# Kernel optimization log

Measured on AMD Instinct MI355X. Metric: run time of the kernel, lower is better.

Reference implementation:

```python
import jax, jax.numpy as jnp
import numpy as np

B, DIM, H, W = 2, 256, 64, 64
HEADS, DIM_HEAD = 8, 64
DIM_INNER = HEADS * DIM_HEAD  # 512


def setup_inputs() -> dict:
    key = jax.random.key(0)
    k1, k2, k3 = jax.random.split(key, 3)
    fmap = jax.random.normal(k1, (B, DIM, H, W), dtype=jnp.float32)
    # 1x1 convs == channel matmuls; store as [out_ch, in_ch]
    w_qkv = jax.random.normal(k2, (3 * DIM_INNER, DIM), dtype=jnp.float32) * (DIM ** -0.5)
    w_out = jax.random.normal(k3, (DIM, DIM_INNER), dtype=jnp.float32) * (DIM_INNER ** -0.5)
    return {"fmap": fmap, "w_qkv": w_qkv, "w_out": w_out}


def reference(fmap, w_qkv, w_out):
    b, c, x, y = fmap.shape
    n = x * y
    h, d = HEADS, DIM_HEAD
    xt = fmap.reshape(b, c, n)                       # [B, C, N]
    qkv = jnp.einsum('oc,bcn->bon', w_qkv, xt)        # [B, 3*h*d, N]
    q, k, v = jnp.split(qkv, 3, axis=1)               # each [B, h*d, N]
    # -> [B, h, N, d]
    to_bhnd = lambda t: t.reshape(b, h, d, n).transpose(0, 1, 3, 2)
    q, k, v = to_bhnd(q), to_bhnd(k), to_bhnd(v)
    # Euclidean distance matrix (torch.cdist p=2)
    q2 = jnp.sum(q * q, axis=-1)                      # [B, h, N]
    k2 = jnp.sum(k * k, axis=-1)                      # [B, h, N]
    qk = jnp.einsum('bhid,bhjd->bhij', q, k)          # [B, h, N, N]
    sim = jnp.sqrt(jnp.maximum(q2[..., :, None] + k2[..., None, :] - 2.0 * qk, 0.0))
    attn = jax.nn.softmax(sim, axis=-1)
    out = jnp.einsum('bhij,bhjd->bhid', attn, v)      # [B, h, N, d]
    out = out.transpose(0, 1, 3, 2).reshape(b, h * d, n)  # [B, h*d, N]
    out = jnp.einsum('oc,bcn->bon', w_out, out)       # [B, dim, N]
    return out.reshape(b, c, x, y)
```

## Files before the change

kernel.cpp:

```cpp
#include <hip/hip_runtime.h>

#define B_      2
#define DIM_    256
#define N_      4096
#define HEADS_  8
#define DINNER_ 512

typedef _Float16 half_t;
typedef _Float16 half8  __attribute__((ext_vector_type(8)));
typedef _Float16 half4v __attribute__((ext_vector_type(4)));
typedef _Float16 half2v __attribute__((ext_vector_type(2)));
typedef float    floatx4 __attribute__((ext_vector_type(4)));

#define SCL_    1.4426950408889634f
#define SHIFT2_ 20.0f


__global__ __launch_bounds__(256) void prep_all(const float* __restrict__ fmap,
                                                const float* __restrict__ w_qkv,
                                                const float* __restrict__ w_out,
                                                half_t* __restrict__ wqF,
                                                half_t* __restrict__ woF,
                                                half_t* __restrict__ xTg) {
    const int t = threadIdx.x, bx = blockIdx.x;
    __shared__ float Tl[64 * 68];
    if (bx < 96) {
        half_t* dst = wqF + (size_t)bx * 4096;
#pragma unroll
        for (int j = 0; j < 2; ++j) {
            const int cch = j * 256 + t;
            const int o = cch >> 4, m15 = cch & 15;
            const float4 a  = *(const float4*)&w_qkv[(size_t)(bx * 16 + m15) * 256 + o * 8];
            const float4 bb = *(const float4*)&w_qkv[(size_t)(bx * 16 + m15) * 256 + o * 8 + 4];
            half8 hv;
            hv[0] = (half_t)a.x;  hv[1] = (half_t)a.y;  hv[2] = (half_t)a.z;  hv[3] = (half_t)a.w;
            hv[4] = (half_t)bb.x; hv[5] = (half_t)bb.y; hv[6] = (half_t)bb.z; hv[7] = (half_t)bb.w;
            *(half8*)(dst + o * 128 + m15 * 8) = hv;
        }
    } else if (bx < 112) {
        const int mt = bx - 96;
        half_t* dst = woF + (size_t)mt * 8192;
#pragma unroll
        for (int j = 0; j < 4; ++j) {
            const int cch = j * 256 + t;
            const int o = cch >> 4, m15 = cch & 15;
            const float4 a  = *(const float4*)&w_out[(size_t)(mt * 16 + m15) * 512 + o * 8];
            const float4 bb = *(const float4*)&w_out[(size_t)(mt * 16 + m15) * 512 + o * 8 + 4];
            half8 hv;
            hv[0] = (half_t)a.x;  hv[1] = (half_t)a.y;  hv[2] = (half_t)a.z;  hv[3] = (half_t)a.w;
            hv[4] = (half_t)bb.x; hv[5] = (half_t)bb.y; hv[6] = (half_t)bb.z; hv[7] = (half_t)bb.w;
            *(half8*)(dst + o * 128 + m15 * 8) = hv;
        }
    } else {
        const int idx = bx - 112;
        const int n0 = (idx & 63) * 64, k0 = ((idx >> 6) & 3) * 64, b = idx >> 8;
        {
            const int kk = t >> 2, nq = (t & 3) * 16;
#pragma unroll
            for (int q = 0; q < 4; ++q) {
                float4 v = *(const float4*)&fmap[((size_t)b * DIM_ + k0 + kk) * N_ + n0 + nq + 4 * q];
                *(float4*)&Tl[kk * 68 + nq + 4 * q] = v;
            }
        }
        __syncthreads();
        {
            const int n = t >> 2, ko = (t & 3) * 16;
            half8 h0, h1;
#pragma unroll
            for (int j = 0; j < 8; ++j) h0[j] = (half_t)Tl[(ko + j) * 68 + n];
#pragma unroll
            for (int j = 0; j < 8; ++j) h1[j] = (half_t)Tl[(ko + 8 + j) * 68 + n];
            half_t* dst = xTg + (((size_t)b * 64 + (n0 >> 6)) * 4 + (k0 >> 6)) * 4096;
            const int o0 = ((ko >> 5) * 4 + (n >> 4)) * 512 + (((ko >> 3) & 3) * 16 + (n & 15)) * 8;
            const int k8 = ko + 8;
            const int o1 = ((k8 >> 5) * 4 + (n >> 4)) * 512 + (((k8 >> 3) & 3) * 16 + (n & 15)) * 8;
            *(half8*)(dst + o0) = h0;
            *(half8*)(dst + o1) = h1;
        }
    }
}

__global__ __launch_bounds__(256) void mm_qkv_mf(const half_t* __restrict__ wqF,
                                                 const half_t* __restrict__ xTg,
                                                 half_t* __restrict__ perm,
                                                 float* __restrict__ sq) {
    const int nt64 = blockIdx.x, by = blockIdx.y, b = blockIdx.z;
    const int t = threadIdx.x, w = t >> 6, L = t & 63, c = L & 15, g = L >> 4;
    const int mt = by * 4 + w;

    const half_t* Ab = wqF + (size_t)mt * 4096;
    const half_t* Bb = xTg + (((size_t)b * 64 + nt64) * 4) * 4096;

    __shared__ __align__(16) char smraw[8192 + 4352];
    half_t* VtH = (half_t*)smraw;
    float*  red = (float*)(smraw + 8192);

    const floatx4 fz = {0.f, 0.f, 0.f, 0.f};
    floatx4 acc[4];
#pragma unroll
    for (int ns = 0; ns < 4; ++ns) acc[ns] = fz;

#pragma unroll
    for (int kc = 0; kc < 8; ++kc) {
        const half8 af = *(const half8*)(Ab + (kc * 4 + g) * 128 + c * 8);
        const half_t* Bs = Bb + (kc >> 1) * 4096 + (kc & 1) * 2048;
#pragma unroll
        for (int ns = 0; ns < 4; ++ns) {
            const half8 bf = *(const half8*)(Bs + ns * 512 + L * 8);
            acc[ns] = __builtin_amdgcn_mfma_f32_16x16x32_f16(af, bf, acc[ns], 0, 0, 0);
        }
    }

    half_t* dst = perm + (((size_t)(b * 24 + by) * 64 + nt64) << 12);
    if (by < 16) {
        float part[4];
#pragma unroll
        for (int ns = 0; ns < 4; ++ns) {
            half_t hv[4];
            float s = 0.f;
#pragma unroll
            for (int i = 0; i < 4; ++i) {
                hv[i] = (half_t)(acc[ns][i] * SCL_);
                const float f = (float)hv[i];
                s = fmaf(f, f, s);
            }
            part[ns] = s;
            const int off = ((w >> 1) * 4 + ns) * 512 + (((2 * w + (g >> 1)) & 3) * 16 + c) * 8 + 4 * (g & 1);
            half2v p0, p1;
            p0[0] = hv[0]; p0[1] = hv[1];
            p1[0] = hv[2]; p1[1] = hv[3];
            *(half2v*)(VtH + off)     = p0;
            *(half2v*)(VtH + off + 2) = p1;
        }
#pragma unroll
        for (int ns = 0; ns < 4; ++ns)
            red[(ns * 16 + (w * 4 + g)) * 17 + c] = part[ns];
        __syncthreads();
#pragma unroll
        for (int j = 0; j < 2; ++j)
            *(half8*)(dst + t * 16 + j * 8) = *(half8*)(VtH + t * 16 + j * 8);
        if (t < 64) {
            const int ns = t >> 4, cc = t & 15;
            float s = 0.f;
#pragma unroll
            for (int wg = 0; wg < 16; ++wg) s += red[(ns * 16 + wg) * 17 + cc];
            const int tens = by >> 3, hh = by & 7;
            sq[((size_t)(tens * 16 + b * 8 + hh)) * N_ + nt64 * 64 + ns * 16 + cc] = s;
        }
    } else {
#pragma unroll
        for (int ns = 0; ns < 4; ++ns)
#pragma unroll
            for (int i = 0; i < 4; ++i)
                VtH[(ns * 4 + w) * 256 + ((c >> 2) * 16 + 4 * g + i) * 4 + (c & 3)] = (half_t)acc[ns][i];
        __syncthreads();
#pragma unroll
        for (int j = 0; j < 2; ++j)
            *(half8*)(dst + t * 16 + j * 8) = *(half8*)(VtH + t * 16 + j * 8);
    }
}

__global__ __launch_bounds__(512) void attn_mfma(const half_t* __restrict__ perm,
                                                 const float* __restrict__ sq,
                                                 half_t* __restrict__ oh,
                                                 float* __restrict__ lbuf) {
    const int bx = blockIdx.x;
    const int qb = bx & 15, kh = bx >> 4;
    const int h = blockIdx.y, b = blockIdx.z;
    const int bh = b * HEADS_ + h;

    const half_t* Qb = perm + ((size_t)(b * 24 + h) << 18);
    const half_t* Kb = perm + ((size_t)(b * 24 + 8 + h) << 18);
    const half_t* Vb = perm + ((size_t)(b * 24 + 16 + h) << 18);
    const float* q2a = sq + (size_t)bh * N_;
    const float* k2a = sq + (size_t)(16 + bh) * N_;

    __shared__ __align__(16) half_t Kl[2][4096];
    __shared__ __align__(16) half_t Vl[2][4096];
    __shared__ __align__(16) float  k2l[1024];

    const int t = threadIdx.x, w = t >> 6, L = t & 63, c = L & 15, g = L >> 4;
    const floatx4 fz = {0.f, 0.f, 0.f, 0.f};

    *(float2*)&k2l[t * 2] = *(const float2*)&k2a[kh * 1024 + t * 2];

    const int tl = w >> 1;
    const int p0 = (w & 1) * 2, p1 = p0 + 1;
    const half_t* Qt = Qb + ((size_t)(qb * 4 + tl) << 12);
    const half8 bq0a = *(const half8*)(Qt + (0 * 4 + p0) * 512 + L * 8);
    const half8 bq1a = *(const half8*)(Qt + (1 * 4 + p0) * 512 + L * 8);
    const half8 bq0b = *(const half8*)(Qt + (0 * 4 + p1) * 512 + L * 8);
    const half8 bq1b = *(const half8*)(Qt + (1 * 4 + p1) * 512 + L * 8);
    const float q2la = q2a[qb * 256 + 64 * tl + 16 * p0 + c];
    const float q2lb = q2a[qb * 256 + 64 * tl + 16 * p1 + c];

    half4v aone;
    {
        const half_t ov = (c == 0) ? (half_t)1.0f : (half_t)0.0f;
        aone[0] = ov; aone[1] = ov; aone[2] = ov; aone[3] = ov;
    }

    floatx4 Oa[4], Ob[4];
    floatx4 laca = fz, lacb = fz;
#pragma unroll
    for (int dt = 0; dt < 4; ++dt) { Oa[dt] = fz; Ob[dt] = fz; }

    const int kt0 = kh * 16;
    half8 rk = *(const half8*)(Kb + ((size_t)kt0 << 12) + t * 8);
    half8 rv = *(const half8*)(Vb + ((size_t)kt0 << 12) + t * 8);

    for (int it = 0; it < 16; ++it) {
        const int buf = it & 1;
        *(half8*)(&Kl[buf][t * 8]) = rk;
        *(half8*)(&Vl[buf][t * 8]) = rv;
        asm volatile("s_waitcnt lgkmcnt(0)\n\ts_barrier" ::: "memory");
        if (it < 15) {
            rk = *(const half8*)(Kb + ((size_t)(kt0 + it + 1) << 12) + t * 8);
            rv = *(const half8*)(Vb + ((size_t)(kt0 + it + 1) << 12) + t * 8);
        }

#pragma unroll
        for (int nt = 0; nt < 4; ++nt) {
            const half8 ak0 = *(const half8*)(&Kl[buf][(0 * 4 + nt) * 512 + L * 8]);
            const half8 ak1 = *(const half8*)(&Kl[buf][(1 * 4 + nt) * 512 + L * 8]);
            floatx4 Sa = __builtin_amdgcn_mfma_f32_16x16x32_f16(ak0, bq0a, fz, 0, 0, 0);
            Sa = __builtin_amdgcn_mfma_f32_16x16x32_f16(ak1, bq1a, Sa, 0, 0, 0);
            floatx4 Sb = __builtin_amdgcn_mfma_f32_16x16x32_f16(ak0, bq0b, fz, 0, 0, 0);
            Sb = __builtin_amdgcn_mfma_f32_16x16x32_f16(ak1, bq1b, Sb, 0, 0, 0);
            const float4 k2v = *(const float4*)&k2l[it * 64 + 16 * nt + 4 * g];

            float pa[4], pb[4];
            const float k2arr[4] = {k2v.x, k2v.y, k2v.z, k2v.w};
#pragma unroll
            for (int i = 0; i < 4; ++i) {
                pa[i] = __builtin_amdgcn_exp2f(
                    __builtin_amdgcn_sqrtf(__builtin_fabsf(fmaf(Sa[i], -2.0f, q2la + k2arr[i]))) - SHIFT2_);
                pb[i] = __builtin_amdgcn_exp2f(
                    __builtin_amdgcn_sqrtf(__builtin_fabsf(fmaf(Sb[i], -2.0f, q2lb + k2arr[i]))) - SHIFT2_);
            }
            half4v bpa, bpb;
            {
                const half2v a0 = __builtin_bit_cast(half2v, __builtin_amdgcn_cvt_pkrtz(pa[0], pa[1]));
                const half2v a1 = __builtin_bit_cast(half2v, __builtin_amdgcn_cvt_pkrtz(pa[2], pa[3]));
                bpa[0] = a0[0]; bpa[1] = a0[1]; bpa[2] = a1[0]; bpa[3] = a1[1];
                const half2v b0 = __builtin_bit_cast(half2v, __builtin_amdgcn_cvt_pkrtz(pb[0], pb[1]));
                const half2v b1 = __builtin_bit_cast(half2v, __builtin_amdgcn_cvt_pkrtz(pb[2], pb[3]));
                bpb[0] = b0[0]; bpb[1] = b0[1]; bpb[2] = b1[0]; bpb[3] = b1[1];
            }

            laca = __builtin_amdgcn_mfma_f32_16x16x16f16(aone, bpa, laca, 0, 0, 0);
            lacb = __builtin_amdgcn_mfma_f32_16x16x16f16(aone, bpb, lacb, 0, 0, 0);
#pragma unroll
            for (int dt = 0; dt < 4; ++dt) {
                const half4v av = *(const half4v*)(&Vl[buf][(nt * 4 + dt) * 256 + L * 4]);
                Oa[dt] = __builtin_amdgcn_mfma_f32_16x16x16f16(av, bpa, Oa[dt], 0, 0, 0);
                Ob[dt] = __builtin_amdgcn_mfma_f32_16x16x16f16(av, bpb, Ob[dt], 0, 0, 0);
            }
        }
    }

    const int ntile = qb * 4 + tl;
    half_t* dst = oh + (size_t)kh * 4194304 + (((size_t)bh * 64 + ntile) << 12);
#pragma unroll
    for (int dt = 0; dt < 4; ++dt) {
        const int obase = ((dt >> 1) * 4) * 512 + (((2 * dt + (g >> 1)) & 3) * 16 + c) * 8 + 4 * (g & 1);
        const half2v a0 = __builtin_bit_cast(half2v, __builtin_amdgcn_cvt_pkrtz(Oa[dt][0], Oa[dt][1]));
        const half2v a1 = __builtin_bit_cast(half2v, __builtin_amdgcn_cvt_pkrtz(Oa[dt][2], Oa[dt][3]));
        *(half2v*)(dst + obase + p0 * 512)     = a0;
        *(half2v*)(dst + obase + p0 * 512 + 2) = a1;
        const half2v b0 = __builtin_bit_cast(half2v, __builtin_amdgcn_cvt_pkrtz(Ob[dt][0], Ob[dt][1]));
        const half2v b1 = __builtin_bit_cast(half2v, __builtin_amdgcn_cvt_pkrtz(Ob[dt][2], Ob[dt][3]));
        *(half2v*)(dst + obase + p1 * 512)     = b0;
        *(half2v*)(dst + obase + p1 * 512 + 2) = b1;
    }
    if (L < 16) {
        const size_t lb0 = (size_t)kh * 65536 + (size_t)bh * N_ + qb * 256 + 64 * tl;
        lbuf[lb0 + 16 * p0 + L] = laca[0];
        lbuf[lb0 + 16 * p1 + L] = lacb[0];
    }
}

__global__ __launch_bounds__(256) void mm_out_mf(const half_t* __restrict__ woF,
                                                 const half_t* __restrict__ oh,
                                                 const float* __restrict__ lbuf,
                                                 float* __restrict__ out) {
    const int nt64 = blockIdx.x, mb = blockIdx.y, b = blockIdx.z;
    const int t = threadIdx.x, w = t >> 6, L = t & 63, c = L & 15, g = L >> 4;
    const int mt = mb * 4 + w;

    const half_t* Ab = woF + (size_t)mt * 8192;
    const floatx4 fz = {0.f, 0.f, 0.f, 0.f};
    floatx4 O4[4];
#pragma unroll
    for (int ns = 0; ns < 4; ++ns) O4[ns] = fz;

#pragma unroll
    for (int h = 0; h < 8; ++h) {
        const int bh = b * 8 + h;
        const size_t toff = (((size_t)bh * 64 + nt64) << 12);
        const half_t* B0 = oh + toff;
        const half_t* B1 = oh + 4194304 + toff;
        const half_t* B2 = oh + 2 * 4194304 + toff;
        const half_t* B3 = oh + 3 * 4194304 + toff;
        floatx4 acc[4];
#pragma unroll
        for (int ns = 0; ns < 4; ++ns) acc[ns] = fz;
#pragma unroll
        for (int c2 = 0; c2 < 2; ++c2) {
            const half8 af = *(const half8*)(Ab + (h * 8 + c2 * 4 + g) * 128 + c * 8);
#pragma unroll
            for (int ns = 0; ns < 4; ++ns) {
                const int boff = (c2 * 4 + ns) * 512 + L * 8;
                const half8 b0 = *(const half8*)(B0 + boff);
                const half8 b1 = *(const half8*)(B1 + boff);
                const half8 b2 = *(const half8*)(B2 + boff);
                const half8 b3 = *(const half8*)(B3 + boff);
                const half8 s = (b0 + b1) + (b2 + b3);
                acc[ns] = __builtin_amdgcn_mfma_f32_16x16x32_f16(af, s, acc[ns], 0, 0, 0);
            }
        }
#pragma unroll
        for (int ns = 0; ns < 4; ++ns) {
            const size_t li = (size_t)bh * N_ + nt64 * 64 + ns * 16 + c;
            const float l = (lbuf[li] + lbuf[65536 + li]) +
                            (lbuf[2 * 65536 + li] + lbuf[3 * 65536 + li]);
            const float inv = __builtin_amdgcn_rcpf(l);
#pragma unroll
            for (int i = 0; i < 4; ++i) O4[ns][i] = fmaf(acc[ns][i], inv, O4[ns][i]);
        }
    }

    float* Cg = out + ((size_t)b * DIM_ + mt * 16) * N_ + nt64 * 64;
#pragma unroll
    for (int ns = 0; ns < 4; ++ns)
#pragma unroll
        for (int i = 0; i < 4; ++i)
            Cg[(size_t)(4 * g + i) * N_ + ns * 16 + c] = O4[ns][i];
}

extern "C" void kernel_launch(void* const* d_in, const int* in_sizes, int n_in,
                              void* d_out, int out_size, void* d_ws, size_t ws_size,
                              hipStream_t stream) {
    const float* fmap  = (const float*)d_in[0];
    const float* w_qkv = (const float*)d_in[1];
    const float* w_out = (const float*)d_in[2];
    float* out = (float*)d_out;

    char* ws = (char*)d_ws;
    half_t* perm = (half_t*)ws;
    float*  sq   = (float*) (ws + 25165824);
    float*  lbuf = (float*) (ws + 25690112);
    half_t* woF  = (half_t*)(ws + 26738688);
    half_t* oh   = (half_t*)(ws + 27000832);
    half_t* xTg  = (half_t*)(ws + 27000832);
    half_t* wqF  = (half_t*)(ws + 31195136);

    prep_all <<<624, 256, 0, stream>>>(fmap, w_qkv, w_out, wqF, woF, xTg);
    mm_qkv_mf<<<dim3(64, 24, 2), 256, 0, stream>>>(wqF, xTg, perm, sq);
    attn_mfma<<<dim3(64, 8, 2), 512, 0, stream>>>(perm, sq, oh, lbuf);
    mm_out_mf<<<dim3(64, 4, 2), 256, 0, stream>>>(woF, oh, lbuf, out);
}
```

Measured before the change: 202.5 us.

## Stage split-K partial reduction in shared memory and prioritize MFMA in attention

In the output projection kernel, the four split-K partial attention outputs and row sums for each head are now loaded cooperatively once per block. They are reduced into a double-buffered LDS tile, with the next head prefetched into registers while the current one is consumed. Previously each of the four waves reloaded and re-summed the same partials from global memory. In the attention kernel, each wave rotates its starting key subtile to spread LDS bank access and wraps MFMA groups in s_setprio to favour matrix issue; this adds barriers and LDS traffic in exchange.

Result: no change. 204.3 us (+0.9%).

```diff
diff --git a/kernel.cpp b/kernel.cpp
--- a/kernel.cpp
+++ b/kernel.cpp
@@ -209,6 +209,8 @@
     half8 rk = *(const half8*)(Kb + ((size_t)kt0 << 12) + t * 8);
     half8 rv = *(const half8*)(Vb + ((size_t)kt0 << 12) + t * 8);
 
+    const int ntrot = w & 3;
+
     for (int it = 0; it < 16; ++it) {
         const int buf = it & 1;
         *(half8*)(&Kl[buf][t * 8]) = rk;
@@ -220,13 +222,16 @@
         }
 
 #pragma unroll
-        for (int nt = 0; nt < 4; ++nt) {
+        for (int ntx = 0; ntx < 4; ++ntx) {
+            const int nt = (ntx + ntrot) & 3;
             const half8 ak0 = *(const half8*)(&Kl[buf][(0 * 4 + nt) * 512 + L * 8]);
             const half8 ak1 = *(const half8*)(&Kl[buf][(1 * 4 + nt) * 512 + L * 8]);
+            __builtin_amdgcn_s_setprio(1);
             floatx4 Sa = __builtin_amdgcn_mfma_f32_16x16x32_f16(ak0, bq0a, fz, 0, 0, 0);
             Sa = __builtin_amdgcn_mfma_f32_16x16x32_f16(ak1, bq1a, Sa, 0, 0, 0);
             floatx4 Sb = __builtin_amdgcn_mfma_f32_16x16x32_f16(ak0, bq0b, fz, 0, 0, 0);
             Sb = __builtin_amdgcn_mfma_f32_16x16x32_f16(ak1, bq1b, Sb, 0, 0, 0);
+            __builtin_amdgcn_s_setprio(0);
             const float4 k2v = *(const float4*)&k2l[it * 64 + 16 * nt + 4 * g];
 
             float pa[4], pb[4];
@@ -248,6 +253,7 @@
                 bpb[0] = b0[0]; bpb[1] = b0[1]; bpb[2] = b1[0]; bpb[3] = b1[1];
             }
 
+            __builtin_amdgcn_s_setprio(1);
             laca = __builtin_amdgcn_mfma_f32_16x16x16f16(aone, bpa, laca, 0, 0, 0);
             lacb = __builtin_amdgcn_mfma_f32_16x16x16f16(aone, bpb, lacb, 0, 0, 0);
 #pragma unroll
@@ -256,6 +262,7 @@
                 Oa[dt] = __builtin_amdgcn_mfma_f32_16x16x16f16(av, bpa, Oa[dt], 0, 0, 0);
                 Ob[dt] = __builtin_amdgcn_mfma_f32_16x16x16f16(av, bpb, Ob[dt], 0, 0, 0);
             }
+            __builtin_amdgcn_s_setprio(0);
         }
     }
 
@@ -294,14 +301,38 @@
 #pragma unroll
     for (int ns = 0; ns < 4; ++ns) O4[ns] = fz;
 
-#pragma unroll
+    __shared__ __align__(16) half_t sh[2][4096];
+    __shared__ float lsh[2][64];
+
+    half8 r0[4], r1[4];
+    float lr[4];
+
+    auto LOADH = [&](int h) {
+        const size_t toff = (((size_t)(b * 8 + h) * 64 + nt64) << 12) + t * 16;
+#pragma unroll
+        for (int q = 0; q < 4; ++q) {
+            r0[q] = *(const half8*)(oh + (size_t)q * 4194304 + toff);
+            r1[q] = *(const half8*)(oh + (size_t)q * 4194304 + toff + 8);
+        }
+        if (t < 64) {
+            const size_t li = (size_t)(b * 8 + h) * N_ + nt64 * 64 + t;
+#pragma unroll
+            for (int q = 0; q < 4; ++q) lr[q] = lbuf[(size_t)q * 65536 + li];
+        }
+    };
+
+    LOADH(0);
     for (int h = 0; h < 8; ++h) {
-        const int bh = b * 8 + h;
-        const size_t toff = (((size_t)bh * 64 + nt64) << 12);
-        const half_t* B0 = oh + toff;
-        const half_t* B1 = oh + 4194304 + toff;
-        const half_t* B2 = oh + 2 * 4194304 + toff;
-        const half_t* B3 = oh + 3 * 4194304 + toff;
+        const int buf = h & 1;
+        const half8 s0 = (r0[0] + r0[1]) + (r0[2] + r0[3]);
+        const half8 s1 = (r1[0] + r1[1]) + (r1[2] + r1[3]);
+        *(half8*)(&sh[buf][t * 16])     = s0;
+        *(half8*)(&sh[buf][t * 16 + 8]) = s1;
+        if (t < 64)
+            lsh[buf][t] = __builtin_amdgcn_rcpf((lr[0] + lr[1]) + (lr[2] + lr[3]));
+        __syncthreads();
+        if (h < 7) LOADH(h + 1);
+
         floatx4 acc[4];
 #pragma unroll
         for (int ns = 0; ns < 4; ++ns) acc[ns] = fz;
@@ -310,21 +341,13 @@
             const half8 af = *(const half8*)(Ab + (h * 8 + c2 * 4 + g) * 128 + c * 8);
 #pragma unroll
             for (int ns = 0; ns < 4; ++ns) {
-                const int boff = (c2 * 4 + ns) * 512 + L * 8;
-                const half8 b0 = *(const half8*)(B0 + boff);
-                const half8 b1 = *(const half8*)(B1 + boff);
-                const half8 b2 = *(const half8*)(B2 + boff);
-                const half8 b3 = *(const half8*)(B3 + boff);
-                const half8 s = (b0 + b1) + (b2 + b3);
-                acc[ns] = __builtin_amdgcn_mfma_f32_16x16x32_f16(af, s, acc[ns], 0, 0, 0);
+                const half8 bf = *(const half8*)(&sh[buf][(c2 * 4 + ns) * 512 + L * 8]);
+                acc[ns] = __builtin_amdgcn_mfma_f32_16x16x32_f16(af, bf, acc[ns], 0, 0, 0);
             }
         }
 #pragma unroll
         for (int ns = 0; ns < 4; ++ns) {
-            const size_t li = (size_t)bh * N_ + nt64 * 64 + ns * 16 + c;
-            const float l = (lbuf[li] + lbuf[65536 + li]) +
-                            (lbuf[2 * 65536 + li] + lbuf[3 * 65536 + li]);
-            const float inv = __builtin_amdgcn_rcpf(l);
+            const float inv = lsh[buf][ns * 16 + c];
 #pragma unroll
             for (int i = 0; i < 4; ++i) O4[ns][i] = fmaf(acc[ns][i], inv, O4[ns][i]);
         }
```
